# Performance work log

Hardware: AMD Instinct MI355X
Metric: run time of the kernel (lower is better)

## Reference

```python
import jax, jax.numpy as jnp
import numpy as np

B, T, N, IN, H, K = 8, 10, 50, 6, 256, 4
E = N * (N - 1)


def setup_inputs() -> dict:
    key = jax.random.key(0)
    ks = jax.random.split(key, 22)
    p = lambda k, shape: jax.random.normal(k, shape, jnp.float32) * 0.05
    return {
        "inputs": jax.random.normal(ks[0], (B, T, N, IN), jnp.float32),
        "sampled_edges": jax.random.uniform(ks[1], (B, T, E, K), dtype=jnp.float32),
        "msg_w1": p(ks[2], (K, H, 2 * H)), "msg_b1": p(ks[3], (K, H)),
        "msg_w2": p(ks[4], (K, H, H)), "msg_b2": p(ks[5], (K, H)),
        "w_hr": p(ks[6], (H, H)), "w_hi": p(ks[7], (H, H)), "w_hh": p(ks[8], (H, H)),
        "w_ir": p(ks[9], (H, IN)), "b_ir": p(ks[10], (H,)),
        "w_ii": p(ks[11], (H, IN)), "b_ii": p(ks[12], (H,)),
        "w_in": p(ks[13], (H, IN)), "b_in": p(ks[14], (H,)),
        "w_o1": p(ks[15], (H, H)), "b_o1": p(ks[16], (H,)),
        "w_o2": p(ks[17], (H, H)), "b_o2": p(ks[18], (H,)),
        "w_o3": p(ks[19], (IN, H)), "b_o3": p(ks[20], (IN,)),
    }


def reference(inputs, sampled_edges, msg_w1, msg_b1, msg_w2, msg_b2,
              w_hr, w_hi, w_hh, w_ir, b_ir, w_ii, b_ii, w_in, b_in,
              w_o1, b_o1, w_o2, b_o2, w_o3, b_o3):
    b, t, n, _ = inputs.shape
    k = msg_w1.shape[0]
    h = msg_w1.shape[1]
    # fully-connected directed graph, no self loops (static indices)
    send_np, recv_np = np.where(np.ones((n, n)) - np.eye(n))
    send = jnp.asarray(send_np)
    recv = jnp.asarray(recv_np)
    norm = float(k) - 1.0  # skip_first_edge_type = True

    def single_step(ins, rel, hidden):
        # ins: [B,N,IN], rel: [B,E,K], hidden: [B,N,H]
        pre = jnp.concatenate([hidden[:, recv], hidden[:, send]], axis=-1)  # [B,E,2H]
        all_msgs = jnp.zeros((b, pre.shape[1], h), inputs.dtype)
        for i in range(1, k):  # skip first edge type
            m = jnp.tanh(jnp.einsum('bef,hf->beh', pre, msg_w1[i]) + msg_b1[i])
            m = jnp.tanh(jnp.einsum('beh,jh->bej', m, msg_w2[i]) + msg_b2[i])
            all_msgs = all_msgs + m * rel[:, :, i:i + 1] / norm
        # scatter-add messages to receiver nodes (replaces onehot matmul)
        agg = jnp.zeros((b, n, h), inputs.dtype).at[:, recv].add(all_msgs) / (n - 1)
        r = jax.nn.sigmoid(ins @ w_ir.T + b_ir + agg @ w_hr.T)
        ig = jax.nn.sigmoid(ins @ w_ii.T + b_ii + agg @ w_hi.T)
        nn_ = jnp.tanh(ins @ w_in.T + b_in + r * (agg @ w_hh.T))
        hidden = (1 - ig) * nn_ + ig * hidden
        pred = jax.nn.relu(hidden @ w_o1.T + b_o1)
        pred = jax.nn.relu(pred @ w_o2.T + b_o2)
        pred = ins + (pred @ w_o3.T + b_o3)
        return pred, hidden

    x_t = jnp.swapaxes(inputs, 0, 1)         # [T,B,N,IN]
    e_t = jnp.swapaxes(sampled_edges, 0, 1)  # [T,B,E,K]
    h0 = jnp.zeros((b, n, h), inputs.dtype)

    def step(carry, xs):
        hidden, prev = carry
        xt, et, s = xs
        ins = jnp.where(s == 0, xt, prev)  # teacher_forcing=False: only step 0 uses inputs
        pred, hidden = single_step(ins, et, hidden)
        return (hidden, pred), pred

    _, preds = jax.lax.scan(step, (h0, jnp.zeros_like(x_t[0])), (x_t, e_t, jnp.arange(t)))
    return jnp.swapaxes(preds, 0, 1)  # [B,T,N,IN]
```

## Files before the change

### kernel.cpp

```cpp
#include <hip/hip_runtime.h>
#include <hip/hip_bf16.h>
#include <stdint.h>

#define B_ 8
#define T_ 10
#define N_ 50
#define IN_ 6
#define H_ 256
#define K_ 4
#define E_ 2450
#define ROWS 400
#define AP 102400

typedef __attribute__((ext_vector_type(8))) __bf16 bf16x8;
typedef __attribute__((ext_vector_type(4))) float f32x4;

__device__ __forceinline__ unsigned short f2bf(float x) {
    unsigned int u = __float_as_uint(x);
    u = (u + 0x7fffu + ((u >> 16) & 1u)) >> 16;
    return (unsigned short)u;
}
__device__ __forceinline__ unsigned pk2(float a, float b) {
    return (unsigned)f2bf(a) | ((unsigned)f2bf(b) << 16);
}
__device__ __forceinline__ float rcp_fast(float x) { return __builtin_amdgcn_rcpf(x); }
__device__ __forceinline__ float tanh_fast(float x) {
    float e = __expf(2.0f * x);
    return 1.0f - 2.0f * rcp_fast(e + 1.0f);
}
__device__ __forceinline__ float sigmoid_fast(float x) {
    return rcp_fast(1.0f + __expf(-x));
}

__global__ __launch_bounds__(256) void swizzle_weights(
        const float* __restrict__ w1, const float* __restrict__ w2,
        const float* __restrict__ whr, const float* __restrict__ whi,
        const float* __restrict__ whh, const float* __restrict__ wo1,
        const float* __restrict__ wo2, const float* __restrict__ b1,
        unsigned short* __restrict__ w1s, unsigned short* __restrict__ w2s,
        unsigned short* __restrict__ gws, unsigned short* __restrict__ wos,
        unsigned int* __restrict__ hidden_zero, float* __restrict__ UV) {
    const int W1N = 3 * 16 * 16 * 64 * 8;
    const int W2N = 3 * 16 * 8 * 64 * 8;
    const int GWN = 3 * 65536;
    const int WON = 2 * 65536;
    const int ZN  = 102400;
    int idx = blockIdx.x * 256 + threadIdx.x;
    if (idx < W1N) {
        int j = idx & 7, L = (idx >> 3) & 63, kt = (idx >> 9) & 15;
        int nt = (idx >> 13) & 15, i = idx >> 17;
        int n = nt * 16 + (L & 15);
        int k = kt * 32 + ((L >> 4) << 3) + j;
        w1s[idx] = f2bf(w1[((size_t)(i + 1) * H_ + n) * (2 * H_) + k]);
    } else if (idx < W1N + W2N) {
        int t = idx - W1N;
        int j = t & 7, L = (t >> 3) & 63, kt = (t >> 9) & 7;
        int nt = (t >> 12) & 15, i = t >> 16;
        int n = nt * 16 + (L & 15);
        int k = kt * 32 + ((L >> 4) << 3) + j;
        w2s[t] = f2bf(w2[((size_t)(i + 1) * H_ + n) * H_ + k]);
    } else if (idx < W1N + W2N + GWN) {
        int t = idx - (W1N + W2N);
        int j = t & 7, L = (t >> 3) & 63, kt = (t >> 9) & 7;
        int nt = (t >> 12) & 15, mat = t >> 16;
        int n = nt * 16 + (L & 15);
        int k = kt * 32 + ((L >> 4) << 3) + j;
        const float* src = (mat == 0) ? whr : (mat == 1) ? whi : whh;
        gws[t] = f2bf(src[(size_t)n * H_ + k]);
    } else if (idx < W1N + W2N + GWN + WON) {
        int t = idx - (W1N + W2N + GWN);
        int j = t & 7, L = (t >> 3) & 63, kt = (t >> 9) & 7;
        int nt = (t >> 12) & 15, g = t >> 16;
        int n = nt * 16 + (L & 15);
        int k = kt * 32 + ((L >> 4) << 3) + j;
        const float* src = (g == 0) ? wo1 : wo2;
        wos[t] = f2bf(src[(size_t)n * H_ + k]);
    } else if (idx < W1N + W2N + GWN + WON + ZN) {
        hidden_zero[idx - (W1N + W2N + GWN + WON)] = 0u;
    } else {
        int t = idx - (W1N + W2N + GWN + WON + ZN);
        int c = t & 511;
        int ty = (t >> 9) % 3;
        UV[t] = (c < 256) ? b1[(ty + 1) * H_ + c] : 0.0f;
    }
}

__global__ __launch_bounds__(256, 4) void msgagg_kernel(
        const float* __restrict__ UV, const float* __restrict__ edges,
        const unsigned short* __restrict__ w2s,
        const float* __restrict__ b2, float* __restrict__ aggP, int t) {
    __shared__ unsigned short m1F[32 * 512];
    __shared__ float relS[64];

    int ty = blockIdx.x / 400;
    int rem = blockIdx.x - ty * 400;
    int b = rem / 50;
    int r = rem - b * 50;
    int tid = threadIdx.x;
    int lane = tid & 63, wid = tid >> 6;
    int col = lane & 15, q = lane >> 4;

    if (tid < 64) {
        float v = 0.0f;
        if (tid < 50 && tid != r) {
            int e = tid * 49 + (r > tid ? r - 1 : r);
            v = edges[(((size_t)b * T_ + t) * E_ + e) * K_ + ty + 1];
        }
        relS[tid] = v;
    }

    {
        int row = wid * 16 + col;
        int sv = row < N_ ? row : N_ - 1;
        const float* Vrow = &UV[((size_t)(b * N_ + sv) * 3 + ty) * 512 + 256 + q * 8];
        const float* Urow = &UV[((size_t)(b * N_ + r) * 3 + ty) * 512 + q * 8];
        #pragma unroll
        for (int kt = 0; kt < 8; ++kt) {
            float4 v0 = *(const float4*)(Vrow + kt * 32);
            float4 v1 = *(const float4*)(Vrow + kt * 32 + 4);
            float4 u0 = *(const float4*)(Urow + kt * 32);
            float4 u1 = *(const float4*)(Urow + kt * 32 + 4);
            float m0 = tanh_fast(u0.x + v0.x);
            float m1 = tanh_fast(u0.y + v0.y);
            float m2 = tanh_fast(u0.z + v0.z);
            float m3 = tanh_fast(u0.w + v0.w);
            float m4 = tanh_fast(u1.x + v1.x);
            float m5 = tanh_fast(u1.y + v1.y);
            float m6 = tanh_fast(u1.z + v1.z);
            float m7 = tanh_fast(u1.w + v1.w);
            uint4 pk;
            pk.x = pk2(m0, m1); pk.y = pk2(m2, m3);
            pk.z = pk2(m4, m5); pk.w = pk2(m6, m7);
            *(uint4*)&m1F[(wid * 8 + kt) * 512 + lane * 8] = pk;
        }
    }
    __syncthreads();

    const bf16x8* w2f = (const bf16x8*)w2s;
    f32x4 acc[4][4];
    #pragma unroll
    for (int mt = 0; mt < 4; ++mt)
        #pragma unroll
        for (int u = 0; u < 4; ++u) acc[mt][u] = (f32x4){0.f, 0.f, 0.f, 0.f};

    #pragma unroll
    for (int kt = 0; kt < 8; ++kt) {
        bf16x8 a0 = *(const bf16x8*)&m1F[(0 * 8 + kt) * 512 + lane * 8];
        bf16x8 a1 = *(const bf16x8*)&m1F[(1 * 8 + kt) * 512 + lane * 8];
        bf16x8 a2 = *(const bf16x8*)&m1F[(2 * 8 + kt) * 512 + lane * 8];
        bf16x8 a3 = *(const bf16x8*)&m1F[(3 * 8 + kt) * 512 + lane * 8];
        #pragma unroll
        for (int u = 0; u < 4; ++u) {
            bf16x8 w = w2f[(size_t)((ty * 16 + wid * 4 + u) * 8 + kt) * 64 + lane];
            acc[0][u] = __builtin_amdgcn_mfma_f32_16x16x32_bf16(a0, w, acc[0][u], 0, 0, 0);
            acc[1][u] = __builtin_amdgcn_mfma_f32_16x16x32_bf16(a1, w, acc[1][u], 0, 0, 0);
            acc[2][u] = __builtin_amdgcn_mfma_f32_16x16x32_bf16(a2, w, acc[2][u], 0, 0, 0);
            acc[3][u] = __builtin_amdgcn_mfma_f32_16x16x32_bf16(a3, w, acc[3][u], 0, 0, 0);
        }
    }
    #pragma unroll
    for (int u = 0; u < 4; ++u) {
        float bias = b2[(ty + 1) * H_ + (wid * 4 + u) * 16 + col];
        float sum = 0.0f;
        #pragma unroll
        for (int mt = 0; mt < 4; ++mt)
            #pragma unroll
            for (int rg = 0; rg < 4; ++rg) {
                int row = mt * 16 + q * 4 + rg;
                sum += tanh_fast(acc[mt][u][rg] + bias) * relS[row];
            }
        sum += __shfl_xor(sum, 16);
        sum += __shfl_xor(sum, 32);
        if (lane < 16)
            aggP[(size_t)ty * AP + (size_t)(b * N_ + r) * H_ +
                 (wid * 4 + u) * 16 + col] = sum * (1.0f / 147.0f);
    }
}

__global__ __launch_bounds__(512) void nodeuv_kernel(
        const float* __restrict__ inputs, const float* __restrict__ aggP,
        const unsigned short* __restrict__ gws, const unsigned short* __restrict__ wos,
        const unsigned short* __restrict__ w1s,
        const float* __restrict__ hid_rd, float* __restrict__ hid_wr,
        float* __restrict__ UV,
        const float* __restrict__ w_ir, const float* __restrict__ b_ir,
        const float* __restrict__ w_ii, const float* __restrict__ b_ii,
        const float* __restrict__ w_in, const float* __restrict__ b_in,
        const float* __restrict__ b1,
        const float* __restrict__ b_o1, const float* __restrict__ b_o2,
        const float* __restrict__ w_o3, const float* __restrict__ b_o3,
        float* __restrict__ out, int t) {
    __shared__ unsigned short aggF[8 * 512];
    __shared__ unsigned short hnF[8 * 512];
    __shared__ unsigned short p1F[8 * 512];
    __shared__ float p2L[16 * 260];
    __shared__ float insS[16 * 6];

    int role = blockIdx.x / 25;
    int mm = blockIdx.x - role * 25;
    if (role > 0 && t == T_ - 1) return;

    int tid = threadIdx.x;
    int lane = tid & 63, wid = tid >> 6;
    int col = lane & 15, q = lane >> 4;

    const float* src = (t == 0) ? inputs : out;
    int tt = (t == 0) ? 0 : (t - 1);

    {
        int kt = tid >> 6, L = tid & 63;
        int row = mm * 16 + (L & 15);
        int k0 = kt * 32 + ((L >> 4) << 3);
        const float* p = &aggP[(size_t)row * H_ + k0];
        float4 a0 = *(const float4*)(p);
        float4 a1 = *(const float4*)(p + 4);
        float4 b0 = *(const float4*)(p + AP);
        float4 b1v = *(const float4*)(p + AP + 4);
        float4 c0 = *(const float4*)(p + 2 * AP);
        float4 c1 = *(const float4*)(p + 2 * AP + 4);
        uint4 pk;
        pk.x = pk2(a0.x + b0.x + c0.x, a0.y + b0.y + c0.y);
        pk.y = pk2(a0.z + b0.z + c0.z, a0.w + b0.w + c0.w);
        pk.z = pk2(a1.x + b1v.x + c1.x, a1.y + b1v.y + c1.y);
        pk.w = pk2(a1.z + b1v.z + c1.z, a1.w + b1v.w + c1.w);
        *(uint4*)&aggF[(size_t)kt * 512 + L * 8] = pk;
    }
    if (tid < 96) {
        int rl = tid / 6, c = tid - rl * 6;
        int row = mm * 16 + rl;
        int b = row / 50, n = row - b * 50;
        insS[rl * 6 + c] = src[(((size_t)b * T_ + tt) * N_ + n) * IN_ + c];
    }
    __syncthreads();

    const bf16x8* gwf = (const bf16x8*)gws;
    bf16x8 af[8];
    #pragma unroll
    for (int kt = 0; kt < 8; ++kt)
        af[kt] = *(const bf16x8*)&aggF[kt * 512 + lane * 8];

    float hpre[2][4];
    #pragma unroll
    for (int u = 0; u < 2; ++u) {
        int h = (wid * 2 + u) * 16 + col;
        #pragma unroll
        for (int rg = 0; rg < 4; ++rg) {
            int row = mm * 16 + q * 4 + rg;
            hpre[u][rg] = hid_rd[(size_t)row * H_ + h];
        }
    }

    const bf16x8* wof = (const bf16x8*)wos;
    const bf16x8* w1f = (const bf16x8*)w1s;
    bf16x8 tw[8][2];
    if (role == 0) {
        #pragma unroll
        for (int kt = 0; kt < 8; ++kt)
            #pragma unroll
            for (int u = 0; u < 2; ++u)
                tw[kt][u] = wof[(size_t)((wid * 2 + u) * 8 + kt) * 64 + lane];
    } else {
        int s = role - 1;
        int ty = s >> 1, half = s & 1;
        #pragma unroll
        for (int kt = 0; kt < 8; ++kt)
            #pragma unroll
            for (int u = 0; u < 2; ++u)
                tw[kt][u] = w1f[(size_t)((ty * 16 + wid * 2 + u) * 16 + half * 8 + kt) * 64 + lane];
    }

    f32x4 acc[3][2];
    #pragma unroll
    for (int m = 0; m < 3; ++m)
        #pragma unroll
        for (int u = 0; u < 2; ++u) acc[m][u] = (f32x4){0.f, 0.f, 0.f, 0.f};

    bf16x8 wg[2][2][3][2];
    #pragma unroll
    for (int ki = 0; ki < 2; ++ki)
        #pragma unroll
        for (int m = 0; m < 3; ++m)
            #pragma unroll
            for (int u = 0; u < 2; ++u)
                wg[0][ki][m][u] = gwf[(size_t)((m * 16 + wid * 2 + u) * 8 + ki) * 64 + lane];
    #pragma unroll
    for (int c = 0; c < 4; ++c) {
        if (c < 3) {
            #pragma unroll
            for (int ki = 0; ki < 2; ++ki)
                #pragma unroll
                for (int m = 0; m < 3; ++m)
                    #pragma unroll
                    for (int u = 0; u < 2; ++u)
                        wg[(c + 1) & 1][ki][m][u] =
                            gwf[(size_t)((m * 16 + wid * 2 + u) * 8 + (c + 1) * 2 + ki) * 64 + lane];
        }
        #pragma unroll
        for (int ki = 0; ki < 2; ++ki)
            #pragma unroll
            for (int m = 0; m < 3; ++m)
                #pragma unroll
                for (int u = 0; u < 2; ++u)
                    acc[m][u] = __builtin_amdgcn_mfma_f32_16x16x32_bf16(
                        af[c * 2 + ki], wg[c & 1][ki][m][u], acc[m][u], 0, 0, 0);
    }

    #pragma unroll
    for (int u = 0; u < 2; ++u) {
        int h = (wid * 2 + u) * 16 + col;
        float bir = b_ir[h], bii = b_ii[h], bin_ = b_in[h];
        float wir[6], wii[6], win[6];
        #pragma unroll
        for (int c = 0; c < 6; ++c) {
            wir[c] = w_ir[h * 6 + c];
            wii[c] = w_ii[h * 6 + c];
            win[c] = w_in[h * 6 + c];
        }
        #pragma unroll
        for (int rg = 0; rg < 4; ++rg) {
            int rl = q * 4 + rg;
            int row = mm * 16 + rl;
            float xr = bir, xi = bii, xn = bin_;
            #pragma unroll
            for (int c = 0; c < 6; ++c) {
                float iv = insS[rl * 6 + c];
                xr += wir[c] * iv;
                xi += wii[c] * iv;
                xn += win[c] * iv;
            }
            float rgate = sigmoid_fast(xr + acc[0][u][rg]);
            float igate = sigmoid_fast(xi + acc[1][u][rg]);
            float nn = tanh_fast(xn + rgate * acc[2][u][rg]);
            float hnew = (1.0f - igate) * nn + igate * hpre[u][rg];
            if (role == 0) hid_wr[(size_t)row * H_ + h] = hnew;
            hnF[(h >> 5) * 512 + (((h >> 3) & 3) * 16 + rl) * 8 + (h & 7)] = f2bf(hnew);
        }
    }
    __syncthreads();

    if (role > 0) {
        int s = role - 1;
        int ty = s >> 1, half = s & 1;
        bf16x8 a2f[8];
        #pragma unroll
        for (int kt = 0; kt < 8; ++kt)
            a2f[kt] = *(const bf16x8*)&hnF[kt * 512 + lane * 8];
        f32x4 acc2[2];
        #pragma unroll
        for (int u = 0; u < 2; ++u) acc2[u] = (f32x4){0.f, 0.f, 0.f, 0.f};
        #pragma unroll
        for (int kt = 0; kt < 8; ++kt)
            #pragma unroll
            for (int u = 0; u < 2; ++u)
                acc2[u] = __builtin_amdgcn_mfma_f32_16x16x32_bf16(a2f[kt], tw[kt][u], acc2[u], 0, 0, 0);
        #pragma unroll
        for (int u = 0; u < 2; ++u) {
            int nt = wid * 2 + u;
            float bias = (half == 0) ? b1[(ty + 1) * H_ + nt * 16 + col] : 0.0f;
            #pragma unroll
            for (int r = 0; r < 4; ++r)
                UV[((size_t)(mm * 16 + q * 4 + r) * 3 + ty) * 512 + half * 256 +
                   nt * 16 + col] = acc2[u][r] + bias;
        }
        return;
    }

    {
        bf16x8 a1f[8];
        #pragma unroll
        for (int kt = 0; kt < 8; ++kt)
            a1f[kt] = *(const bf16x8*)&hnF[kt * 512 + lane * 8];
        bf16x8 o2w[8][2];
        #pragma unroll
        for (int kt = 0; kt < 8; ++kt)
            #pragma unroll
            for (int u = 0; u < 2; ++u)
                o2w[kt][u] = wof[(size_t)((16 + wid * 2 + u) * 8 + kt) * 64 + lane];
        f32x4 a1v[2];
        #pragma unroll
        for (int u = 0; u < 2; ++u) a1v[u] = (f32x4){0.f, 0.f, 0.f, 0.f};
        #pragma unroll
        for (int kt = 0; kt < 8; ++kt)
            #pragma unroll
            for (int u = 0; u < 2; ++u)
                a1v[u] = __builtin_amdgcn_mfma_f32_16x16x32_bf16(a1f[kt], tw[kt][u], a1v[u], 0, 0, 0);
        #pragma unroll
        for (int u = 0; u < 2; ++u) {
            int h = (wid * 2 + u) * 16 + col;
            float bo = b_o1[h];
            #pragma unroll
            for (int rg = 0; rg < 4; ++rg) {
                int rl = q * 4 + rg;
                float v = fmaxf(a1v[u][rg] + bo, 0.0f);
                p1F[(h >> 5) * 512 + (((h >> 3) & 3) * 16 + rl) * 8 + (h & 7)] = f2bf(v);
            }
        }
        __syncthreads();

        bf16x8 a2f[8];
        #pragma unroll
        for (int kt = 0; kt < 8; ++kt)
            a2f[kt] = *(const bf16x8*)&p1F[kt * 512 + lane * 8];
        f32x4 a2v[2];
        #pragma unroll
        for (int u = 0; u < 2; ++u) a2v[u] = (f32x4){0.f, 0.f, 0.f, 0.f};
        #pragma unroll
        for (int kt = 0; kt < 8; ++kt)
            #pragma unroll
            for (int u = 0; u < 2; ++u)
                a2v[u] = __builtin_amdgcn_mfma_f32_16x16x32_bf16(a2f[kt], o2w[kt][u], a2v[u], 0, 0, 0);
        #pragma unroll
        for (int u = 0; u < 2; ++u) {
            int h = (wid * 2 + u) * 16 + col;
            float bo = b_o2[h];
            #pragma unroll
            for (int rg = 0; rg < 4; ++rg) {
                int rl = q * 4 + rg;
                p2L[rl * 260 + h] = fmaxf(a2v[u][rg] + bo, 0.0f);
            }
        }
    }
    __syncthreads();

    if (tid < 192) {
        int o = tid >> 3;
        int part = tid & 7;
        #pragma unroll
        for (int pass = 0; pass < 4; ++pass) {
            int oo = o + pass * 24;
            int rl = oo / 6, c = oo - rl * 6;
            float acc3 = (part == 0) ? b_o3[c] : 0.0f;
            const float* wrow = &w_o3[c * 256];
            const float* prow = &p2L[rl * 260];
            #pragma unroll
            for (int i = 0; i < 8; ++i) {
                int k = i * 32 + part * 4;
                float4 w = *(const float4*)&wrow[k];
                float4 p = *(const float4*)&prow[k];
                acc3 += w.x * p.x + w.y * p.y + w.z * p.z + w.w * p.w;
            }
            acc3 += __shfl_xor(acc3, 1);
            acc3 += __shfl_xor(acc3, 2);
            acc3 += __shfl_xor(acc3, 4);
            if (part == 0) {
                int row = mm * 16 + rl;
                int b = row / 50, n = row - b * 50;
                out[(((size_t)b * T_ + t) * N_ + n) * IN_ + c] = insS[rl * 6 + c] + acc3;
            }
        }
    }
}

extern "C" void kernel_launch(void* const* d_in, const int* in_sizes, int n_in,
                              void* d_out, int out_size, void* d_ws, size_t ws_size,
                              hipStream_t stream) {
    const float* inputs = (const float*)d_in[0];
    const float* edges  = (const float*)d_in[1];
    const float* msg_w1 = (const float*)d_in[2];
    const float* msg_b1 = (const float*)d_in[3];
    const float* msg_w2 = (const float*)d_in[4];
    const float* msg_b2 = (const float*)d_in[5];
    const float* w_hr = (const float*)d_in[6];
    const float* w_hi = (const float*)d_in[7];
    const float* w_hh = (const float*)d_in[8];
    const float* w_ir = (const float*)d_in[9];
    const float* b_ir = (const float*)d_in[10];
    const float* w_ii = (const float*)d_in[11];
    const float* b_ii = (const float*)d_in[12];
    const float* w_in = (const float*)d_in[13];
    const float* b_in = (const float*)d_in[14];
    const float* w_o1 = (const float*)d_in[15];
    const float* b_o1 = (const float*)d_in[16];
    const float* w_o2 = (const float*)d_in[17];
    const float* b_o2 = (const float*)d_in[18];
    const float* w_o3 = (const float*)d_in[19];
    const float* b_o3 = (const float*)d_in[20];
    float* out = (float*)d_out;

    char* ws = (char*)d_ws;
    float* hidden0           = (float*)(ws);
    float* hidden1           = (float*)(ws + 409600);
    float* UV                = (float*)(ws + 819200);
    float* aggP              = (float*)(ws + 3276800);
    unsigned short* w1s      = (unsigned short*)(ws + 4505600);
    unsigned short* w2s      = (unsigned short*)(ws + 5292032);
    unsigned short* gws      = (unsigned short*)(ws + 5685248);
    unsigned short* wos      = (unsigned short*)(ws + 6078464);

    swizzle_weights<<<dim3(6384), dim3(256), 0, stream>>>(
        msg_w1, msg_w2, w_hr, w_hi, w_hh, w_o1, w_o2, msg_b1,
        w1s, w2s, gws, wos, (unsigned int*)hidden0, UV);

    float* hid[2] = {hidden0, hidden1};
    for (int t = 0; t < T_; ++t) {
        msgagg_kernel<<<dim3(1200), dim3(256), 0, stream>>>(
            UV, edges, w2s, msg_b2, aggP, t);
        nodeuv_kernel<<<dim3(175), dim3(512), 0, stream>>>(
            inputs, aggP, gws, wos, w1s, hid[t & 1], hid[(t + 1) & 1], UV,
            w_ir, b_ir, w_ii, b_ii, w_in, b_in, msg_b1,
            b_o1, b_o2, w_o3, b_o3, out, t);
    }
}
```

Before: 487.3 us.

## Fuse edge-type loop into msgagg and emit bf16 MFMA-layout aggregate

The message kernel now loops over the three edge types inside one block per (batch, receiver) and accumulates their weighted sums in registers, instead of launching one block per edge type and writing three fp32 partial buffers. The result is written directly as bf16 in the fragment layout nodeuv expects, so nodeuv loads its A fragments straight from global memory and skips the reduce-and-pack pass and its shared buffer. This removes partial-buffer traffic and a sync, but cuts msgagg's grid from 1200 to 400 blocks, which lowers parallelism on a GPU with many CUs and serialises the three types within a block.

```diff
diff --git a/kernel.cpp b/kernel.cpp
--- a/kernel.cpp
+++ b/kernel.cpp
@@ -88,97 +88,110 @@
 __global__ __launch_bounds__(256, 4) void msgagg_kernel(
         const float* __restrict__ UV, const float* __restrict__ edges,
         const unsigned short* __restrict__ w2s,
-        const float* __restrict__ b2, float* __restrict__ aggP, int t) {
+        const float* __restrict__ b2, unsigned short* __restrict__ aggB, int t) {
     __shared__ unsigned short m1F[32 * 512];
-    __shared__ float relS[64];
-
-    int ty = blockIdx.x / 400;
-    int rem = blockIdx.x - ty * 400;
-    int b = rem / 50;
-    int r = rem - b * 50;
+    __shared__ float relS[3][64];
+
+    int b = blockIdx.x / 50;
+    int r = blockIdx.x - b * 50;
     int tid = threadIdx.x;
     int lane = tid & 63, wid = tid >> 6;
     int col = lane & 15, q = lane >> 4;
 
     if (tid < 64) {
-        float v = 0.0f;
+        float v0 = 0.f, v1 = 0.f, v2 = 0.f;
         if (tid < 50 && tid != r) {
             int e = tid * 49 + (r > tid ? r - 1 : r);
-            v = edges[(((size_t)b * T_ + t) * E_ + e) * K_ + ty + 1];
-        }
-        relS[tid] = v;
-    }
-
-    {
-        int row = wid * 16 + col;
-        int sv = row < N_ ? row : N_ - 1;
-        const float* Vrow = &UV[((size_t)(b * N_ + sv) * 3 + ty) * 512 + 256 + q * 8];
-        const float* Urow = &UV[((size_t)(b * N_ + r) * 3 + ty) * 512 + q * 8];
+            const float* ep = &edges[(((size_t)b * T_ + t) * E_ + e) * K_];
+            v0 = ep[1]; v1 = ep[2]; v2 = ep[3];
+        }
+        relS[0][tid] = v0; relS[1][tid] = v1; relS[2][tid] = v2;
+    }
+
+    const bf16x8* w2f = (const bf16x8*)w2s;
+    float sumAcc[4] = {0.f, 0.f, 0.f, 0.f};
+
+    for (int ty = 0; ty < 3; ++ty) {
+        {
+            int row = wid * 16 + col;
+            int sv = row < N_ ? row : N_ - 1;
+            const float* Vrow = &UV[((size_t)(b * N_ + sv) * 3 + ty) * 512 + 256 + q * 8];
+            const float* Urow = &UV[((size_t)(b * N_ + r) * 3 + ty) * 512 + q * 8];
+            #pragma unroll
+            for (int kt = 0; kt < 8; ++kt) {
+                float4 v0 = *(const float4*)(Vrow + kt * 32);
+                float4 v1 = *(const float4*)(Vrow + kt * 32 + 4);
+                float4 u0 = *(const float4*)(Urow + kt * 32);
+                float4 u1 = *(const float4*)(Urow + kt * 32 + 4);
+                float m0 = tanh_fast(u0.x + v0.x);
+                float m1 = tanh_fast(u0.y + v0.y);
+                float m2 = tanh_fast(u0.z + v0.z);
+                float m3 = tanh_fast(u0.w + v0.w);
+                float m4 = tanh_fast(u1.x + v1.x);
+                float m5 = tanh_fast(u1.y + v1.y);
+                float m6 = tanh_fast(u1.z + v1.z);
+                float m7 = tanh_fast(u1.w + v1.w);
+                uint4 pk;
+                pk.x = pk2(m0, m1); pk.y = pk2(m2, m3);
+                pk.z = pk2(m4, m5); pk.w = pk2(m6, m7);
+                *(uint4*)&m1F[(wid * 8 + kt) * 512 + lane * 8] = pk;
+            }
+        }
+        __syncthreads();
+
+        f32x4 acc[4][4];
+        #pragma unroll
+        for (int mt = 0; mt < 4; ++mt)
+            #pragma unroll
+            for (int u = 0; u < 4; ++u) acc[mt][u] = (f32x4){0.f, 0.f, 0.f, 0.f};
+
         #pragma unroll
         for (int kt = 0; kt < 8; ++kt) {
-            float4 v0 = *(const float4*)(Vrow + kt * 32);
-            float4 v1 = *(const float4*)(Vrow + kt * 32 + 4);
-            float4 u0 = *(const float4*)(Urow + kt * 32);
-            float4 u1 = *(const float4*)(Urow + kt * 32 + 4);
-            float m0 = tanh_fast(u0.x + v0.x);
-            float m1 = tanh_fast(u0.y + v0.y);
-            float m2 = tanh_fast(u0.z + v0.z);
-            float m3 = tanh_fast(u0.w + v0.w);
-            float m4 = tanh_fast(u1.x + v1.x);
-            float m5 = tanh_fast(u1.y + v1.y);
-            float m6 = tanh_fast(u1.z + v1.z);
-            float m7 = tanh_fast(u1.w + v1.w);
-            uint4 pk;
-            pk.x = pk2(m0, m1); pk.y = pk2(m2, m3);
-            pk.z = pk2(m4, m5); pk.w = pk2(m6, m7);
-            *(uint4*)&m1F[(wid * 8 + kt) * 512 + lane * 8] = pk;
-        }
-    }
-    __syncthreads();
-
-    const bf16x8* w2f = (const bf16x8*)w2s;
-    f32x4 acc[4][4];
-    #pragma unroll
-    for (int mt = 0; mt < 4; ++mt)
-        #pragma unroll
-        for (int u = 0; u < 4; ++u) acc[mt][u] = (f32x4){0.f, 0.f, 0.f, 0.f};
-
-    #pragma unroll
-    for (int kt = 0; kt < 8; ++kt) {
-        bf16x8 a0 = *(const bf16x8*)&m1F[(0 * 8 + kt) * 512 + lane * 8];
-        bf16x8 a1 = *(const bf16x8*)&m1F[(1 * 8 + kt) * 512 + lane * 8];
-        bf16x8 a2 = *(const bf16x8*)&m1F[(2 * 8 + kt) * 512 + lane * 8];
-        bf16x8 a3 = *(const bf16x8*)&m1F[(3 * 8 + kt) * 512 + lane * 8];
+            bf16x8 a0 = *(const bf16x8*)&m1F[(0 * 8 + kt) * 512 + lane * 8];
+            bf16x8 a1 = *(const bf16x8*)&m1F[(1 * 8 + kt) * 512 + lane * 8];
+            bf16x8 a2 = *(const bf16x8*)&m1F[(2 * 8 + kt) * 512 + lane * 8];
+            bf16x8 a3 = *(const bf16x8*)&m1F[(3 * 8 + kt) * 512 + lane * 8];
+            #pragma unroll
+            for (int u = 0; u < 4; ++u) {
+                bf16x8 w = w2f[(size_t)((ty * 16 + wid * 4 + u) * 8 + kt) * 64 + lane];
+                acc[0][u] = __builtin_amdgcn_mfma_f32_16x16x32_bf16(a0, w, acc[0][u], 0, 0, 0);
+                acc[1][u] = __builtin_amdgcn_mfma_f32_16x16x32_bf16(a1, w, acc[1][u], 0, 0, 0);
+                acc[2][u] = __builtin_amdgcn_mfma_f32_16x16x32_bf16(a2, w, acc[2][u], 0, 0, 0);
+                acc[3][u] = __builtin_amdgcn_mfma_f32_16x16x32_bf16(a3, w, acc[3][u], 0, 0, 0);
+            }
+        }
         #pragma unroll
         for (int u = 0; u < 4; ++u) {
-            bf16x8 w = w2f[(size_t)((ty * 16 + wid * 4 + u) * 8 + kt) * 64 + lane];
-            acc[0][u] = __builtin_amdgcn_mfma_f32_16x16x32_bf16(a0, w, acc[0][u], 0, 0, 0);
-            acc[1][u] = __builtin_amdgcn_mfma_f32_16x16x32_bf16(a1, w, acc[1][u], 0, 0, 0);
-            acc[2][u] = __builtin_amdgcn_mfma_f32_16x16x32_bf16(a2, w, acc[2][u], 0, 0, 0);
-            acc[3][u] = __builtin_amdgcn_mfma_f32_16x16x32_bf16(a3, w, acc[3][u], 0, 0, 0);
-        }
-    }
+            float bias = b2[(ty + 1) * H_ + (wid * 4 + u) * 16 + col];
+            #pragma unroll
+            for (int mt = 0; mt < 4; ++mt)
+                #pragma unroll
+                for (int rg = 0; rg < 4; ++rg) {
+                    int row = mt * 16 + q * 4 + rg;
+                    sumAcc[u] += tanh_fast(acc[mt][u][rg] + bias) * relS[ty][row];
+                }
+        }
+        __syncthreads();
+    }
+
+    int rr = b * 50 + r;
+    int mm = rr >> 4, rl = rr & 15;
     #pragma unroll
     for (int u = 0; u < 4; ++u) {
-        float bias = b2[(ty + 1) * H_ + (wid * 4 + u) * 16 + col];
-        float sum = 0.0f;
-        #pragma unroll
-        for (int mt = 0; mt < 4; ++mt)
-            #pragma unroll
-            for (int rg = 0; rg < 4; ++rg) {
-                int row = mt * 16 + q * 4 + rg;
-                sum += tanh_fast(acc[mt][u][rg] + bias) * relS[row];
-            }
-        sum += __shfl_xor(sum, 16);
-        sum += __shfl_xor(sum, 32);
-        if (lane < 16)
-            aggP[(size_t)ty * AP + (size_t)(b * N_ + r) * H_ +
-                 (wid * 4 + u) * 16 + col] = sum * (1.0f / 147.0f);
+        float s = sumAcc[u];
+        s += __shfl_xor(s, 16);
+        s += __shfl_xor(s, 32);
+        if (lane < 16) {
+            int h = (wid * 4 + u) * 16 + col;
+            int kt = h >> 5;
+            aggB[(size_t)mm * 4096 + kt * 512 + (((h >> 3) & 3) * 16 + rl) * 8 + (h & 7)]
+                = f2bf(s * (1.0f / 147.0f));
+        }
     }
 }
 
 __global__ __launch_bounds__(512) void nodeuv_kernel(
-        const float* __restrict__ inputs, const float* __restrict__ aggP,
+        const float* __restrict__ inputs, const unsigned short* __restrict__ aggB,
         const unsigned short* __restrict__ gws, const unsigned short* __restrict__ wos,
         const unsigned short* __restrict__ w1s,
         const float* __restrict__ hid_rd, float* __restrict__ hid_wr,
@@ -190,7 +203,6 @@
         const float* __restrict__ b_o1, const float* __restrict__ b_o2,
         const float* __restrict__ w_o3, const float* __restrict__ b_o3,
         float* __restrict__ out, int t) {
-    __shared__ unsigned short aggF[8 * 512];
     __shared__ unsigned short hnF[8 * 512];
     __shared__ unsigned short p1F[8 * 512];
     __shared__ float p2L[16 * 260];
@@ -207,37 +219,17 @@
     const float* src = (t == 0) ? inputs : out;
     int tt = (t == 0) ? 0 : (t - 1);
 
-    {
-        int kt = tid >> 6, L = tid & 63;
-        int row = mm * 16 + (L & 15);
-        int k0 = kt * 32 + ((L >> 4) << 3);
-        const float* p = &aggP[(size_t)row * H_ + k0];
-        float4 a0 = *(const float4*)(p);
-        float4 a1 = *(const float4*)(p + 4);
-        float4 b0 = *(const float4*)(p + AP);
-        float4 b1v = *(const float4*)(p + AP + 4);
-        float4 c0 = *(const float4*)(p + 2 * AP);
-        float4 c1 = *(const float4*)(p + 2 * AP + 4);
-        uint4 pk;
-        pk.x = pk2(a0.x + b0.x + c0.x, a0.y + b0.y + c0.y);
-        pk.y = pk2(a0.z + b0.z + c0.z, a0.w + b0.w + c0.w);
-        pk.z = pk2(a1.x + b1v.x + c1.x, a1.y + b1v.y + c1.y);
-        pk.w = pk2(a1.z + b1v.z + c1.z, a1.w + b1v.w + c1.w);
-        *(uint4*)&aggF[(size_t)kt * 512 + L * 8] = pk;
-    }
     if (tid < 96) {
         int rl = tid / 6, c = tid - rl * 6;
         int row = mm * 16 + rl;
         int b = row / 50, n = row - b * 50;
         insS[rl * 6 + c] = src[(((size_t)b * T_ + tt) * N_ + n) * IN_ + c];
     }
-    __syncthreads();
-
-    const bf16x8* gwf = (const bf16x8*)gws;
+
     bf16x8 af[8];
     #pragma unroll
     for (int kt = 0; kt < 8; ++kt)
-        af[kt] = *(const bf16x8*)&aggF[kt * 512 + lane * 8];
+        af[kt] = *(const bf16x8*)&aggB[(size_t)mm * 4096 + kt * 512 + lane * 8];
 
     float hpre[2][4];
     #pragma unroll
@@ -269,6 +261,7 @@
                 tw[kt][u] = w1f[(size_t)((ty * 16 + wid * 2 + u) * 16 + half * 8 + kt) * 64 + lane];
     }
 
+    const bf16x8* gwf = (const bf16x8*)gws;
     f32x4 acc[3][2];
     #pragma unroll
     for (int m = 0; m < 3; ++m)
@@ -304,6 +297,7 @@
                     acc[m][u] = __builtin_amdgcn_mfma_f32_16x16x32_bf16(
                         af[c * 2 + ki], wg[c & 1][ki][m][u], acc[m][u], 0, 0, 0);
     }
+    __syncthreads();
 
     #pragma unroll
     for (int u = 0; u < 2; ++u) {
@@ -481,7 +475,7 @@
     float* hidden0           = (float*)(ws);
     float* hidden1           = (float*)(ws + 409600);
     float* UV                = (float*)(ws + 819200);
-    float* aggP              = (float*)(ws + 3276800);
+    unsigned short* aggB     = (unsigned short*)(ws + 3276800);
     unsigned short* w1s      = (unsigned short*)(ws + 4505600);
     unsigned short* w2s      = (unsigned short*)(ws + 5292032);
     unsigned short* gws      = (unsigned short*)(ws + 5685248);
@@ -493,10 +487,10 @@
 
     float* hid[2] = {hidden0, hidden1};
     for (int t = 0; t < T_; ++t) {
-        msgagg_kernel<<<dim3(1200), dim3(256), 0, stream>>>(
-            UV, edges, w2s, msg_b2, aggP, t);
+        msgagg_kernel<<<dim3(400), dim3(256), 0, stream>>>(
+            UV, edges, w2s, msg_b2, aggB, t);
         nodeuv_kernel<<<dim3(175), dim3(512), 0, stream>>>(
-            inputs, aggP, gws, wos, w1s, hid[t & 1], hid[(t + 1) & 1], UV,
+            inputs, aggB, gws, wos, w1s, hid[t & 1], hid[(t + 1) & 1], UV,
             w_ir, b_ir, w_ii, b_ii, w_in, b_in, msg_b1,
             b_o1, b_o2, w_o3, b_o3, out, t);
     }
```

Result: slower. 723.5 us (+48.5%).
